# Optimization experiments

Measured on AMD Instinct MI355X. Metric: run time of the kernel, lower is better.

## Reference

```python
import jax, jax.numpy as jnp
import numpy as np

N = 100000   # nodes
K = 32       # fixed neighbor count per node
IN_C = 128
OUT_C = 64


def setup_inputs() -> dict:
    key = jax.random.key(0)
    k1, k2, k3 = jax.random.split(key, 3)
    x = jax.random.normal(k1, (N, IN_C), dtype=jnp.float32)
    nbrs = jax.random.randint(k2, (N, K), 0, N, dtype=jnp.int64)
    # nn.Linear weight [out, in], no bias
    W = jax.random.normal(k3, (OUT_C, IN_C), dtype=jnp.float32) * (1.0 / np.sqrt(IN_C))
    return {"x": x, "nbrs": nbrs, "W": W}


def reference(x, nbrs, W):
    # h = self.w(x): [N, out]
    h = jnp.einsum("ni,oi->no", x, W)
    # gather neighbor features: [N, K, out]
    gathered = h[nbrs]
    # torch.median(dim=0): lower middle element of sorted values (no averaging)
    med_idx = (K - 1) // 2
    out = jnp.sort(gathered, axis=1)[:, med_idx, :]  # [N, out]
    return out
```

## Files before the change

kernel.cpp:

```cpp
#include <hip/hip_runtime.h>
#include <hip/hip_fp16.h>

#define NNODES 100000
#define KNBR 32
#define IN_C 128
#define OUT_C 64


typedef __attribute__((ext_vector_type(8))) short bf16x8;
typedef __attribute__((ext_vector_type(4))) float f32x4;

__device__ __forceinline__ unsigned short bf16_rne(float f) {
    unsigned u = __builtin_bit_cast(unsigned, f);
    u = (u + 0x7FFFu + ((u >> 16) & 1u)) >> 16;
    return (unsigned short)u;
}
__device__ __forceinline__ float bf16_f(unsigned short s) {
    unsigned u = ((unsigned)s) << 16;
    return __builtin_bit_cast(float, u);
}

__device__ __forceinline__ void split8(const float4& u, const float4& v,
                                       bf16x8& hi, bf16x8& lo) {
    const float f[8] = {u.x, u.y, u.z, u.w, v.x, v.y, v.z, v.w};
#pragma unroll
    for (int j = 0; j < 8; ++j) {
        const unsigned short hb = bf16_rne(f[j]);
        hi[j] = (short)hb;
        lo[j] = (short)bf16_rne(f[j] - bf16_f(hb));
    }
}

#define GW_LD 136

__global__ __launch_bounds__(256) void gemm_h_kernel(
    const float* __restrict__ x, const float* __restrict__ W,
    __half* __restrict__ h)
{
    __shared__ __align__(16) unsigned short swh[64 * GW_LD];
    __shared__ __align__(16) unsigned short swl[64 * GW_LD];

    const int t = threadIdx.x;

#pragma unroll
    for (int i = 0; i < 8; ++i) {
        const int e   = t + 256 * i;
        const int row = e >> 5;
        const int c4  = (e & 31) * 4;
        const float4 wv = *(const float4*)(W + row * IN_C + c4);
        ushort4 ph, pl;
        ph.x = bf16_rne(wv.x); pl.x = bf16_rne(wv.x - bf16_f(ph.x));
        ph.y = bf16_rne(wv.y); pl.y = bf16_rne(wv.y - bf16_f(ph.y));
        ph.z = bf16_rne(wv.z); pl.z = bf16_rne(wv.z - bf16_f(ph.z));
        ph.w = bf16_rne(wv.w); pl.w = bf16_rne(wv.w - bf16_f(ph.w));
        *(ushort4*)(swh + row * GW_LD + c4) = ph;
        *(ushort4*)(swl + row * GW_LD + c4) = pl;
    }
    __syncthreads();

    const int lane = t & 63;
    const int w    = t >> 6;
    const int r    = lane & 15;
    const int g    = lane >> 4;
    const int nb   = blockIdx.x * 128 + 32 * w;

    f32x4 acc[2][4];
#pragma unroll
    for (int i = 0; i < 2; ++i)
#pragma unroll
        for (int c = 0; c < 4; ++c) acc[i][c] = (f32x4){0.f, 0.f, 0.f, 0.f};

    int n0 = nb + r;       if (n0 > NNODES - 1) n0 = NNODES - 1;
    int n1 = nb + 16 + r;  if (n1 > NNODES - 1) n1 = NNODES - 1;
    const float* px0 = x + (size_t)n0 * IN_C;
    const float* px1 = x + (size_t)n1 * IN_C;

#pragma unroll
    for (int ks = 0; ks < 4; ++ks) {
        const int k0 = 32 * ks + 8 * g;
        const float4 u0 = *(const float4*)(px0 + k0);
        const float4 v0 = *(const float4*)(px0 + k0 + 4);
        const float4 u1 = *(const float4*)(px1 + k0);
        const float4 v1 = *(const float4*)(px1 + k0 + 4);
        bf16x8 a0h, a0l, a1h, a1l;
        split8(u0, v0, a0h, a0l);
        split8(u1, v1, a1h, a1l);
#pragma unroll
        for (int c = 0; c < 4; ++c) {
            const int wrow = 16 * c + r;
            const bf16x8 bh = *(const bf16x8*)(swh + wrow * GW_LD + k0);
            const bf16x8 bl = *(const bf16x8*)(swl + wrow * GW_LD + k0);
            acc[0][c] = __builtin_amdgcn_mfma_f32_16x16x32_bf16(a0h, bh, acc[0][c], 0, 0, 0);
            acc[1][c] = __builtin_amdgcn_mfma_f32_16x16x32_bf16(a1h, bh, acc[1][c], 0, 0, 0);
            acc[0][c] = __builtin_amdgcn_mfma_f32_16x16x32_bf16(a0l, bh, acc[0][c], 0, 0, 0);
            acc[1][c] = __builtin_amdgcn_mfma_f32_16x16x32_bf16(a1l, bh, acc[1][c], 0, 0, 0);
            acc[0][c] = __builtin_amdgcn_mfma_f32_16x16x32_bf16(a0h, bl, acc[0][c], 0, 0, 0);
            acc[1][c] = __builtin_amdgcn_mfma_f32_16x16x32_bf16(a1h, bl, acc[1][c], 0, 0, 0);
        }
    }

#pragma unroll
    for (int rf = 0; rf < 2; ++rf) {
#pragma unroll
        for (int i = 0; i < 4; ++i) {
            const int node = nb + 16 * rf + 4 * g + i;
            if (node < NNODES) {
                __half* ph = h + (size_t)node * OUT_C + r;
#pragma unroll
                for (int c = 0; c < 4; ++c)
                    ph[16 * c] = __float2half(acc[rf][c][i]);
            }
        }
    }
}

__device__ __forceinline__ unsigned pk_min(unsigned a, unsigned b) {
    unsigned d;
    asm("v_pk_min_f16 %0, %1, %2" : "=v"(d) : "v"(a), "v"(b));
    return d;
}
__device__ __forceinline__ unsigned pk_max(unsigned a, unsigned b) {
    unsigned d;
    asm("v_pk_max_f16 %0, %1, %2" : "=v"(d) : "v"(a), "v"(b));
    return d;
}
__device__ __forceinline__ void ce(unsigned& a, unsigned& b) {
    const unsigned lo = pk_min(a, b);
    b = pk_max(a, b);
    a = lo;
}

__device__ __forceinline__ void sort16(unsigned* v) {
    constexpr unsigned char net[63][2] = {
        {0,1},{2,3},{4,5},{6,7},{8,9},{10,11},{12,13},{14,15},
        {0,2},{1,3},{4,6},{5,7},{8,10},{9,11},{12,14},{13,15},
        {1,2},{5,6},{9,10},{13,14},
        {0,4},{1,5},{2,6},{3,7},{8,12},{9,13},{10,14},{11,15},
        {2,4},{3,5},{10,12},{11,13},
        {1,2},{3,4},{5,6},{9,10},{11,12},{13,14},
        {0,8},{1,9},{2,10},{3,11},{4,12},{5,13},{6,14},{7,15},
        {4,8},{5,9},{6,10},{7,11},
        {2,4},{3,5},{6,8},{7,9},{10,12},{11,13},
        {1,2},{3,4},{5,6},{7,8},{9,10},{11,12},{13,14}
    };
#pragma unroll
    for (int i = 0; i < 63; ++i) ce(v[net[i][0]], v[net[i][1]]);
}

__device__ __forceinline__ unsigned median32(unsigned* v) {
    sort16(v);
    sort16(v + 16);
    const unsigned* A = v;
    const unsigned* B = v + 16;
    const unsigned e2a = pk_max(pk_max(A[0], B[0]), pk_min(A[8],  B[8]));
    const unsigned o1a = pk_min(pk_max(A[4], B[4]), pk_min(A[12], B[12]));
    const unsigned Ep4 = pk_max(e2a, o1a);
    const unsigned e2b = pk_max(pk_max(A[2], B[2]), pk_min(A[10], B[10]));
    const unsigned o1b = pk_min(pk_max(A[6], B[6]), pk_min(A[14], B[14]));
    const unsigned Op3 = pk_min(e2b, o1b);
    const unsigned E8  = pk_max(Ep4, Op3);
    const unsigned e2c = pk_max(pk_max(A[1], B[1]), pk_min(A[9],  B[9]));
    const unsigned o1c = pk_min(pk_max(A[5], B[5]), pk_min(A[13], B[13]));
    const unsigned Ep4o = pk_max(e2c, o1c);
    const unsigned e2d = pk_max(pk_max(A[3], B[3]), pk_min(A[11], B[11]));
    const unsigned o1d = pk_min(pk_max(A[7], B[7]), pk_min(A[15], B[15]));
    const unsigned Op3o = pk_min(e2d, o1d);
    const unsigned O7  = pk_min(Ep4o, Op3o);
    return pk_min(E8, O7);
}

__global__ __launch_bounds__(256) void median_kernel(
    const __half* __restrict__ h, const int* __restrict__ nbrs,
    float* __restrict__ out)
{
    const int t = threadIdx.x;
    const int li   = t & 31;
    const int node = blockIdx.x * 8 + (t >> 5);

    const int idx  = nbrs[node * KNBR + li];
    const int bval = idx << 7;
    const int gbase = (t & 32) << 2;
    const unsigned chb = (unsigned)li << 2;

    const unsigned char* hb = (const unsigned char*)h;

    unsigned ro[KNBR];
#pragma unroll
    for (int k = 0; k < KNBR; ++k)
        ro[k] = (unsigned)__builtin_amdgcn_ds_bpermute(gbase + 4 * k, bval) + chb;
    __builtin_amdgcn_sched_barrier(0);

    unsigned a[KNBR];
#pragma unroll
    for (int k = 0; k < KNBR; ++k)
        a[k] = *(const unsigned*)(hb + ro[k]);
    __builtin_amdgcn_sched_barrier(0);

    const unsigned m = median32(a);
    const __half2 hm = *(const __half2*)&m;
    float2 o;
    o.x = __low2float(hm);
    o.y = __high2float(hm);
    *(float2*)(out + node * OUT_C + 2 * li) = o;
}

extern "C" void kernel_launch(void* const* d_in, const int* in_sizes, int n_in,
                              void* d_out, int out_size, void* d_ws, size_t ws_size,
                              hipStream_t stream) {
    (void)in_sizes; (void)n_in; (void)out_size; (void)ws_size;
    const float* x    = (const float*)d_in[0];
    const int*   nbrs = (const int*)d_in[1];
    const float* W    = (const float*)d_in[2];
    float* out = (float*)d_out;
    __half* h  = (__half*)d_ws;

    gemm_h_kernel<<<(NNODES + 127) / 128, 256, 0, stream>>>(x, W, h);
    median_kernel<<<NNODES / 8, 256, 0, stream>>>(h, nbrs, out);
}
```

Measured before the change: 147.0 us.

## Split h into two channel-half planes and process median per half

The GEMM now writes h as two separate planes of 32 channels each (N x 32 halves) instead of one interleaved N x 64 array. The median kernel runs two block ranges, one per plane, with 16 threads per node, so each plane (about 6.4 MB) is more likely to stay resident in cache during the random neighbor gather. In exchange each node's neighbor indices are read twice, the gathers become 64-byte rows instead of 128-byte rows, and the sched_barriers around the gather were removed.

```diff
diff --git a/kernel.cpp b/kernel.cpp
--- a/kernel.cpp
+++ b/kernel.cpp
@@ -5,6 +5,7 @@
 #define KNBR 32
 #define IN_C 128
 #define OUT_C 64
+#define HALF_BLOCKS 6250
 
 
 typedef __attribute__((ext_vector_type(8))) short bf16x8;
@@ -105,10 +106,11 @@
         for (int i = 0; i < 4; ++i) {
             const int node = nb + 16 * rf + 4 * g + i;
             if (node < NNODES) {
-                __half* ph = h + (size_t)node * OUT_C + r;
-#pragma unroll
-                for (int c = 0; c < 4; ++c)
-                    ph[16 * c] = __float2half(acc[rf][c][i]);
+#pragma unroll
+                for (int c = 0; c < 4; ++c) {
+                    h[(size_t)(c >> 1) * (NNODES * 32) + (size_t)node * 32
+                      + 16 * (c & 1) + r] = __float2half(acc[rf][c][i]);
+                }
             }
         }
     }
@@ -174,34 +176,39 @@
     float* __restrict__ out)
 {
     const int t = threadIdx.x;
-    const int li   = t & 31;
-    const int node = blockIdx.x * 8 + (t >> 5);
-
-    const int idx  = nbrs[node * KNBR + li];
-    const int bval = idx << 7;
-    const int gbase = (t & 32) << 2;
+    const int li   = t & 15;
+    const int half = blockIdx.x / HALF_BLOCKS;
+    const int node = (blockIdx.x % HALF_BLOCKS) * 16 + (t >> 4);
+
+    const unsigned char* hb =
+        (const unsigned char*)(h + (size_t)half * (NNODES * 32));
+
+    const int idx0 = nbrs[node * KNBR + li];
+    const int idx1 = nbrs[node * KNBR + 16 + li];
+    const int bv0 = idx0 << 6;
+    const int bv1 = idx1 << 6;
+    const int gbase = (t & 48) << 2;
     const unsigned chb = (unsigned)li << 2;
 
-    const unsigned char* hb = (const unsigned char*)h;
-
     unsigned ro[KNBR];
 #pragma unroll
-    for (int k = 0; k < KNBR; ++k)
-        ro[k] = (unsigned)__builtin_amdgcn_ds_bpermute(gbase + 4 * k, bval) + chb;
-    __builtin_amdgcn_sched_barrier(0);
+    for (int k = 0; k < 16; ++k)
+        ro[k] = (unsigned)__builtin_amdgcn_ds_bpermute(gbase + 4 * k, bv0) + chb;
+#pragma unroll
+    for (int k = 0; k < 16; ++k)
+        ro[16 + k] = (unsigned)__builtin_amdgcn_ds_bpermute(gbase + 4 * k, bv1) + chb;
 
     unsigned a[KNBR];
 #pragma unroll
     for (int k = 0; k < KNBR; ++k)
         a[k] = *(const unsigned*)(hb + ro[k]);
-    __builtin_amdgcn_sched_barrier(0);
 
     const unsigned m = median32(a);
     const __half2 hm = *(const __half2*)&m;
     float2 o;
     o.x = __low2float(hm);
     o.y = __high2float(hm);
-    *(float2*)(out + node * OUT_C + 2 * li) = o;
+    *(float2*)(out + node * OUT_C + half * 32 + 2 * li) = o;
 }
 
 extern "C" void kernel_launch(void* const* d_in, const int* in_sizes, int n_in,
@@ -215,5 +222,5 @@
     __half* h  = (__half*)d_ws;
 
     gemm_h_kernel<<<(NNODES + 127) / 128, 256, 0, stream>>>(x, W, h);
-    median_kernel<<<NNODES / 8, 256, 0, stream>>>(h, nbrs, out);
-}
+    median_kernel<<<2 * HALF_BLOCKS, 256, 0, stream>>>(h, nbrs, out);
+}
```

New measurement: 156.4 us. 1.06x slower.
